# Kernel optimization log

Measured on AMD Instinct MI355X. Metric: run time of the kernel, lower is better.

## Reference

```python
import jax, jax.numpy as jnp
import numpy as np

N, L, S = 512, 1024, 32   # batch, latent dim, spatial (S*S == L)
F = 32 * S * S            # flattened encoder conv features (last conv = 32 ch)
H = 512                   # hidden width of latent MLP heads


def _lrelu(x):
    return jnp.where(x >= 0, x, 0.01 * x)


def _bn(x):
    # BatchNorm2d in training mode, gamma=1, beta=0 (default init)
    m = x.mean((0, 2, 3), keepdims=True)
    v = x.var((0, 2, 3), keepdims=True)
    return (x - m) * jax.lax.rsqrt(v + 1e-5)


def _conv(x, w, b):
    y = jax.lax.conv_general_dilated(x, w, (1, 1), 'SAME',
                                     dimension_numbers=('NCHW', 'OIHW', 'NCHW'))
    return y + b[None, :, None, None]


def _block(x, w, b):
    return _lrelu(_bn(_conv(x, w, b)))


def setup_inputs() -> dict:
    key = jax.random.key(0)
    ks = jax.random.split(key, 16)
    r = lambda k, s, sc: jax.random.normal(k, s, jnp.float32) * sc
    return {
        'x': r(ks[0], (N, 1, S, S), 1.0),
        'eps_c': r(ks[1], (N, L), 1.0),
        'eps_s': r(ks[2], (N, L), 1.0),
        'enc_cw1': r(ks[3], (2, 32, 1, 3, 3), 0.1),   'enc_cb1': jnp.zeros((2, 32)),
        'enc_cw2': r(ks[4], (2, 64, 32, 3, 3), 0.05), 'enc_cb2': jnp.zeros((2, 64)),
        'enc_cw3': r(ks[5], (2, 32, 64, 3, 3), 0.05), 'enc_cb3': jnp.zeros((2, 32)),
        'enc_muW1': r(ks[6], (2, H, F), 0.005), 'enc_muB1': jnp.zeros((2, H)),
        'enc_muW2': r(ks[7], (2, L, H), 0.02),  'enc_muB2': jnp.zeros((2, L)),
        'enc_vaW1': r(ks[8], (2, H, F), 0.005), 'enc_vaB1': jnp.zeros((2, H)),
        'enc_vaW2': r(ks[9], (2, L, H), 0.02),  'enc_vaB2': jnp.zeros((2, L)),
        'dec_cw1': r(ks[10], (2, 32, 1, 3, 3), 0.1),   'dec_cb1': jnp.zeros((2, 32)),
        'dec_cw2': r(ks[11], (2, 64, 32, 3, 3), 0.05), 'dec_cb2': jnp.zeros((2, 64)),
        'dec_cw3': r(ks[12], (2, 1, 64, 3, 3), 0.05),  'dec_cb3': jnp.zeros((2, 1)),
    }


def reference(x, eps_c, eps_s,
              enc_cw1, enc_cb1, enc_cw2, enc_cb2, enc_cw3, enc_cb3,
              enc_muW1, enc_muB1, enc_muW2, enc_muB2,
              enc_vaW1, enc_vaB1, enc_vaW2, enc_vaB2,
              dec_cw1, dec_cb1, dec_cw2, dec_cb2, dec_cw3, dec_cb3):
    def encode(i):
        h = _block(x, enc_cw1[i], enc_cb1[i])
        h = _block(h, enc_cw2[i], enc_cb2[i])
        h = _block(h, enc_cw3[i], enc_cb3[i])
        f = h.reshape(N, -1)                                   # [N, F]
        mu = _lrelu(_lrelu(f @ enc_muW1[i].T + enc_muB1[i]) @ enc_muW2[i].T + enc_muB2[i])
        lv = _lrelu(_lrelu(f @ enc_vaW1[i].T + enc_vaB1[i]) @ enc_vaW2[i].T + enc_vaB2[i])
        return mu, lv                                          # each [N, L]

    def decode(z, i):
        h = z.reshape(N, 1, S, S)
        h = _block(h, dec_cw1[i], dec_cb1[i])
        h = _block(h, dec_cw2[i], dec_cb2[i])
        h = _block(h, dec_cw3[i], dec_cb3[i])
        return h.reshape(N, 1, S, S)

    class_mu, class_logvar = encode(0)
    style_mu, style_logvar = encode(1)

    # precision-weighted product-of-experts group evidence (vectorized)
    precision = jnp.exp(-style_logvar)                  # 1/var, [N, L]
    group_var = 1.0 / precision.sum(0)                  # [L]
    group_mu = (style_mu * precision).sum(0) * group_var  # [L]
    group_logvar = jnp.log(group_var)

    # reparameterize
    z_c = eps_c * jnp.exp(0.5 * class_logvar) + class_mu          # [N, L]
    z_s = eps_s * jnp.exp(0.5 * group_logvar)[None] + group_mu[None]  # [N, L]

    output_c = decode(z_c, 0)
    output_s = jax.nn.relu(decode(z_s, 1))
    output = output_c * output_s                        # [N, 1, S, S]

    kl1 = -0.5 * jnp.sum(1.0 + class_logvar) + 0.5 * (
        jnp.sum(class_mu ** 2) + jnp.sum(jnp.exp(class_logvar) ** 2))
    kl2 = -0.5 * jnp.sum(1.0 + group_logvar) + 0.5 * (
        jnp.sum(group_mu ** 2) + jnp.sum(jnp.exp(group_logvar) ** 2))
    recon = (jnp.exp(x) - jnp.exp(output)) ** 2
    loss = -kl1 + kl2 + recon                           # [N, 1, S, S]
    return loss, output
```

## Files before the change

kernel.cpp:

```cpp
#include <hip/hip_runtime.h>

constexpr int N_   = 512;
constexpr int PIX  = 1024;
constexpr int L_   = 1024;
constexpr int F_   = 32768;
constexpr int H_   = 512;
constexpr float IC_ = 1.0f / (float)(512 * 1024);

__device__ __forceinline__ float lrelu(float t) { return t >= 0.f ? t : 0.01f * t; }

using frag  = __attribute__((ext_vector_type(8))) short;
using f32x4 = __attribute__((ext_vector_type(4))) float;
using s4    = __attribute__((ext_vector_type(4))) short;

__device__ __forceinline__ void split_bf16(float v, short& hi, short& lo) {
    const unsigned b = __float_as_uint(v);
    hi = (short)(b >> 16);
    const float hf = __uint_as_float(b & 0xFFFF0000u);
    lo = (short)(__float_as_uint(v - hf) >> 16);
}

__device__ __forceinline__ frag ld2(const short* p) {
    union { frag f; struct { unsigned long long a, b; } u; } x;
    x.u.a = *(const unsigned long long*)(p);
    x.u.b = *(const unsigned long long*)(p + 4);
    return x.f;
}

__global__ __launch_bounds__(256) void wsplit6_kernel(
    const float* __restrict__ w0, const float* __restrict__ w1,
    const float* __restrict__ w2, const float* __restrict__ w3,
    const float* __restrict__ w4, const float* __restrict__ w5,
    short* __restrict__ hi, short* __restrict__ lo)
{
    const int layer = blockIdx.y;
    const float* W = layer == 0 ? w0 : layer == 1 ? w1 : layer == 2 ? w2 :
                     layer == 3 ? w3 : layer == 4 ? w4 : w5;
    const int CIN  = (layer == 1 || layer == 3) ? 64 : 32;
    const int NCOT = (layer == 1 || layer == 3) ? 2 : 4;
    const int idx = blockIdx.x * 256 + threadIdx.x;
    const int j    = idx & 7;
    const int lane = (idx >> 3) & 63;
    const int q    = lane >> 4, lm = lane & 15;
    const int blk  = idx >> 9;
    const int cot  = blk % NCOT;
    const int rest = blk / NCOT;
    const int pos  = rest % 9;
    const int cc   = rest / 9;
    const int co = cot * 16 + lm;
    const int ci = cc * 32 + q * 8 + j;
    short h, l;
    split_bf16(W[((size_t)co * CIN + ci) * 9 + pos], h, l);
    hi[layer * 18432 + idx] = h;
    lo[layer * 18432 + idx] = l;
}

template<int CIN, int COUT, bool BN_IN>
__global__ __launch_bounds__(256) void conv_mfma(
    const float* __restrict__ in, const short* __restrict__ wh,
    const short* __restrict__ wl, const float* __restrict__ bias,
    float* __restrict__ out, const float* __restrict__ stats_in,
    float* __restrict__ stats_out)
{
    constexpr int NCOT = COUT / 16;
    constexpr int NCH  = CIN / 32;
    constexpr int STR  = 36;
    constexpr int PLsh = 340 * STR;
    __shared__ __align__(16) short hiL[PLsh];
    __shared__ __align__(16) short loL[PLsh];
    __shared__ float red[2 * COUT];
    __shared__ float bnm[64], bni[64];
    const int tid  = threadIdx.x;
    const int n    = blockIdx.x >> 2;
    const int y0   = (blockIdx.x & 3) << 3;
    const int lane = tid & 63;
    const int wv   = tid >> 6;
    const int lm   = lane & 15;
    const int q    = lane >> 4;

    if (tid < 2 * COUT) red[tid] = 0.f;
    if (BN_IN && tid < CIN) {
        const float m  = stats_in[tid] * IC_;
        const float qq = stats_in[CIN + tid] * IC_;
        bnm[tid] = m;
        bni[tid] = rsqrtf(qq - m * m + 1e-5f);
    }
    __syncthreads();

    f32x4 acc[NCOT][4];
#pragma unroll
    for (int t = 0; t < NCOT; ++t)
#pragma unroll
        for (int pt = 0; pt < 4; ++pt) acc[t][pt] = {0.f, 0.f, 0.f, 0.f};

    const int rs0 = tid / 34, cs0 = tid % 34;
    const int idx1 = tid + 256;
    const int rs1 = idx1 / 34, cs1 = idx1 % 34;
    const int gr0 = y0 - 1 + rs0, gc0 = cs0 - 1;
    const int gr1 = y0 - 1 + rs1, gc1 = cs1 - 1;
    const bool in1 = idx1 < 340;
    const bool ok0 = ((unsigned)gr0 < 32u) && ((unsigned)gc0 < 32u);
    const bool ok1 = in1 && ((unsigned)gr1 < 32u) && ((unsigned)gc1 < 32u);
    const int  po0 = gr0 * 32 + gc0;
    const int  po1 = gr1 * 32 + gc1;

    const float* inb = in + ((size_t)n * CIN << 10);

    frag ahA[NCOT], alA[NCOT], ahB[NCOT], alB[NCOT];

    auto LDW = [&](frag (&dh)[NCOT], frag (&dl)[NCOT], int posAbs) {
#pragma unroll
        for (int t = 0; t < NCOT; ++t) {
            const size_t wb = (size_t)((posAbs * NCOT + t) * 512 + lane * 8);
            dh[t] = *(const frag*)&wh[wb];
            dl[t] = *(const frag*)&wl[wb];
        }
    };

    auto COMPUTE = [&](int pos, frag (&fh)[NCOT], frag (&fl)[NCOT]) {
        const int ky = pos / 3, kx = pos - ky * 3;
        __builtin_amdgcn_s_setprio(1);
#pragma unroll
        for (int pt = 0; pt < 4; ++pt) {
            const int ptile = wv * 4 + pt;
            const int row = ptile >> 1;
            const int col = ((ptile & 1) << 4) + lm;
            const int loff = ((row + ky) * 34 + col + kx) * STR + q * 8;
            const frag bh = ld2(&hiL[loff]);
            const frag bl = ld2(&loL[loff]);
#pragma unroll
            for (int t = 0; t < NCOT; ++t) {
                acc[t][pt] = __builtin_amdgcn_mfma_f32_16x16x32_bf16(
                    fh[t], bh, acc[t][pt], 0, 0, 0);
                acc[t][pt] = __builtin_amdgcn_mfma_f32_16x16x32_bf16(
                    fh[t], bl, acc[t][pt], 0, 0, 0);
                acc[t][pt] = __builtin_amdgcn_mfma_f32_16x16x32_bf16(
                    fl[t], bh, acc[t][pt], 0, 0, 0);
            }
        }
        __builtin_amdgcn_s_setprio(0);
    };

#pragma unroll 1
    for (int cc = 0; cc < NCH; ++cc) {
        if (cc) __syncthreads();

        LDW(ahA, alA, cc * 9 + 0);

        {
            float v0r[32], v1r[32];
#pragma unroll
            for (int u = 0; u < 32; ++u) {
                const int cg = cc * 32 + u;
                v0r[u] = ok0 ? inb[((size_t)cg << 10) + po0] : 0.f;
                v1r[u] = ok1 ? inb[((size_t)cg << 10) + po1] : 0.f;
            }
#pragma unroll
            for (int u4 = 0; u4 < 32; u4 += 4) {
                s4 h0v, l0v, h1v, l1v;
#pragma unroll
                for (int e = 0; e < 4; ++e) {
                    const int ci = u4 + e;
                    const int cg = cc * 32 + ci;
                    float v0 = v0r[ci];
                    if (BN_IN && ok0) v0 = lrelu((v0 - bnm[cg]) * bni[cg]);
                    short h, l;
                    split_bf16(v0, h, l);
                    h0v[e] = h; l0v[e] = l;
                    float v1 = v1r[ci];
                    if (BN_IN && ok1) v1 = lrelu((v1 - bnm[cg]) * bni[cg]);
                    short h1, l1;
                    split_bf16(v1, h1, l1);
                    h1v[e] = h1; l1v[e] = l1;
                }
                *(s4*)&hiL[tid * STR + u4] = h0v;
                *(s4*)&loL[tid * STR + u4] = l0v;
                if (in1) {
                    *(s4*)&hiL[idx1 * STR + u4] = h1v;
                    *(s4*)&loL[idx1 * STR + u4] = l1v;
                }
            }
        }
        __syncthreads();

#pragma unroll 1
        for (int pos = 0; pos < 8; pos += 2) {
            LDW(ahB, alB, cc * 9 + pos + 1);
            COMPUTE(pos, ahA, alA);
            LDW(ahA, alA, cc * 9 + pos + 2);
            COMPUTE(pos + 1, ahB, alB);
        }
        COMPUTE(8, ahA, alA);
    }

    float* ob = out + ((size_t)n * COUT << 10);
#pragma unroll
    for (int t = 0; t < NCOT; ++t) {
#pragma unroll
        for (int r = 0; r < 4; ++r) {
            const int co = t * 16 + q * 4 + r;
            const float b = bias[co];
            float s = 0.f, sq = 0.f;
#pragma unroll
            for (int pt = 0; pt < 4; ++pt) {
                const float v = acc[t][pt][r] + b;
                ob[((size_t)co << 10) + (y0 << 5) + ((wv * 4 + pt) << 4) + lm] = v;
                s += v; sq += v * v;
            }
#pragma unroll
            for (int off = 8; off > 0; off >>= 1) {
                s  += __shfl_down(s, off, 64);
                sq += __shfl_down(sq, off, 64);
            }
            if (lm == 0) {
                atomicAdd(&red[co], s);
                atomicAdd(&red[COUT + co], sq);
            }
        }
    }
    __syncthreads();
    if (tid < 2 * COUT) atomicAdd(&stats_out[tid], red[tid]);
}

template<int CIN, int COPB, bool BN_IN>
__global__ __launch_bounds__(256) void conv3x3(
    const float* __restrict__ in, const float* __restrict__ w,
    const float* __restrict__ bias, float* __restrict__ out,
    const float* __restrict__ stats_in, float* __restrict__ stats_out,
    int Cout)
{
    constexpr int CT = (CIN < 4) ? CIN : 4;
    __shared__ float tile[CT * PIX];
    __shared__ float red[2 * COPB];
    const int groups = Cout / COPB;
    const int n   = blockIdx.x / groups;
    const int co0 = (blockIdx.x % groups) * COPB;
    const int tid = threadIdx.x;
    const int x   = tid & 31;
    const int y0  = (tid >> 5) * 4;

    float acc[COPB][4];
#pragma unroll
    for (int c = 0; c < COPB; ++c)
#pragma unroll
        for (int j = 0; j < 4; ++j) acc[c][j] = 0.f;

    const float* inbase = in + (size_t)n * CIN * PIX;

#pragma unroll 1
    for (int s0 = 0; s0 < CIN; s0 += CT) {
        __syncthreads();
#pragma unroll
        for (int s = 0; s < CT; ++s) {
            float4 v = ((const float4*)(inbase + (size_t)(s0 + s) * PIX))[tid];
            if (BN_IN) {
                const int c = s0 + s;
                const float m   = stats_in[c] * IC_;
                const float q   = stats_in[CIN + c] * IC_;
                const float inv = rsqrtf(q - m * m + 1e-5f);
                v.x = lrelu((v.x - m) * inv);
                v.y = lrelu((v.y - m) * inv);
                v.z = lrelu((v.z - m) * inv);
                v.w = lrelu((v.w - m) * inv);
            }
            ((float4*)tile)[s * 256 + tid] = v;
        }
        __syncthreads();
#pragma unroll 2
        for (int s = 0; s < CT; ++s) {
            const int ci = s0 + s;
            const float* tp = tile + s * PIX;
            float r[6][3];
#pragma unroll
            for (int ry = 0; ry < 6; ++ry) {
                const int yy = y0 + ry - 1;
                const bool yok = (unsigned)yy < 32u;
#pragma unroll
                for (int cx = 0; cx < 3; ++cx) {
                    const int xx = x + cx - 1;
                    const bool ok = yok && ((unsigned)xx < 32u);
                    r[ry][cx] = ok ? tp[yy * 32 + xx] : 0.f;
                }
            }
#pragma unroll
            for (int c = 0; c < COPB; ++c) {
                const float* wp = w + ((size_t)(co0 + c) * CIN + ci) * 9;
#pragma unroll
                for (int ky = 0; ky < 3; ++ky)
#pragma unroll
                    for (int kx = 0; kx < 3; ++kx) {
                        const float wv = wp[ky * 3 + kx];
#pragma unroll
                        for (int j = 0; j < 4; ++j)
                            acc[c][j] += r[ky + j][kx] * wv;
                    }
            }
        }
    }

    if (tid < 2 * COPB) red[tid] = 0.f;
    __syncthreads();
#pragma unroll
    for (int c = 0; c < COPB; ++c) {
        const float b = bias[co0 + c];
        float* ob = out + (((size_t)n * Cout + co0 + c) << 10);
        float s = 0.f, q = 0.f;
#pragma unroll
        for (int j = 0; j < 4; ++j) {
            const float v = acc[c][j] + b;
            ob[(y0 + j) * 32 + x] = v;
            s += v; q += v * v;
        }
#pragma unroll
        for (int off = 32; off > 0; off >>= 1) {
            s += __shfl_down(s, off, 64);
            q += __shfl_down(q, off, 64);
        }
        if ((tid & 63) == 0) {
            atomicAdd(&red[c], s);
            atomicAdd(&red[COPB + c], q);
        }
    }
    __syncthreads();
    if (tid < COPB)
        atomicAdd(&stats_out[co0 + tid], red[tid]);
    else if (tid < 2 * COPB)
        atomicAdd(&stats_out[Cout + co0 + tid - COPB], red[tid]);
}

template<bool BN_A>
__global__ __launch_bounds__(256) void gemm_mfma(
    const float* __restrict__ A0, const float* __restrict__ A1,
    const float* __restrict__ B0, const float* __restrict__ B1,
    float* __restrict__ C0, float* __restrict__ C1,
    int K, int Nh, int kchunk, int xph,
    const float* __restrict__ bnstats, int Cin)
{
    __shared__ short AhL[4096], AlL[4096], BhL[4096], BlL[4096];
    const int tid  = threadIdx.x;
    const int head = blockIdx.x / xph;
    const int n0   = (blockIdx.x % xph) * 128;
    const int m0   = blockIdx.y * 128;
    const float* A = head ? A1 : A0;
    const float* B = head ? B1 : B0;
    float*       C = head ? C1 : C0;
    const int k0 = blockIdx.z * kchunk;
    const int k1 = k0 + kchunk;

    const int lane = tid & 63;
    const int wv   = tid >> 6;
    const int wm   = wv & 1;
    const int wn   = wv >> 1;
    const int lm   = lane & 15;
    const int q    = lane >> 4;

    const int srow = tid >> 1;
    const int smt  = srow >> 4;
    const int slm  = srow & 15;
    const int sq0  = (tid & 1) * 2;
    const int ks   = (tid & 1) * 16;

    float bn_m = 0.f, bn_inv = 1.f;
    if (BN_A) {
        const int c = k0 >> 10;
        bn_m = bnstats[c] * IC_;
        const float qq = bnstats[Cin + c] * IC_;
        bn_inv = rsqrtf(qq - bn_m * bn_m + 1e-5f);
    }

    f32x4 acc[4][4];
#pragma unroll
    for (int i = 0; i < 4; ++i)
#pragma unroll
        for (int j = 0; j < 4; ++j) acc[i][j] = {0.f, 0.f, 0.f, 0.f};

    auto cv8 = [](float4 u, float4 w2, frag& h, frag& l) {
        const float v[8] = {u.x, u.y, u.z, u.w, w2.x, w2.y, w2.z, w2.w};
#pragma unroll
        for (int e = 0; e < 8; ++e) {
            short hh, ll;
            split_bf16(v[e], hh, ll);
            h[e] = hh; l[e] = ll;
        }
    };

    float4 a4[4], b4[4];
    auto LOADAB = [&](int kb) {
        const float* Ap = A + (size_t)(m0 + srow) * K + kb + ks;
        const float* Bp = B + (size_t)(n0 + srow) * K + kb + ks;
#pragma unroll
        for (int g = 0; g < 4; ++g) a4[g] = ((const float4*)Ap)[g];
#pragma unroll
        for (int g = 0; g < 4; ++g) b4[g] = ((const float4*)Bp)[g];
    };

    LOADAB(k0);

#pragma unroll 1
    for (int kb = k0; kb < k1; kb += 32) {
        if (BN_A) {
#pragma unroll
            for (int g = 0; g < 4; ++g) {
                a4[g].x = lrelu((a4[g].x - bn_m) * bn_inv);
                a4[g].y = lrelu((a4[g].y - bn_m) * bn_inv);
                a4[g].z = lrelu((a4[g].z - bn_m) * bn_inv);
                a4[g].w = lrelu((a4[g].w - bn_m) * bn_inv);
            }
        }

        frag ah0, al0, ah1, al1, bh0, bl0, bh1, bl1;
        cv8(a4[0], a4[1], ah0, al0);
        cv8(a4[2], a4[3], ah1, al1);
        cv8(b4[0], b4[1], bh0, bl0);
        cv8(b4[2], b4[3], bh1, bl1);

        __syncthreads();
        const int o0 = ((smt * 4 + sq0) * 16 + slm) * 8;
        const int o1 = ((smt * 4 + sq0 + 1) * 16 + slm) * 8;
        *(frag*)&AhL[o0] = ah0;  *(frag*)&AhL[o1] = ah1;
        *(frag*)&AlL[o0] = al0;  *(frag*)&AlL[o1] = al1;
        *(frag*)&BhL[o0] = bh0;  *(frag*)&BhL[o1] = bh1;
        *(frag*)&BlL[o0] = bl0;  *(frag*)&BlL[o1] = bl1;
        __syncthreads();

        frag fah[4], fal[4], fbh[4], fbl[4];
#pragma unroll
        for (int t = 0; t < 4; ++t) {
            const int oa = (((wm * 4 + t) * 4 + q) * 16 + lm) * 8;
            const int ob = (((wn * 4 + t) * 4 + q) * 16 + lm) * 8;
            fah[t] = *(const frag*)&AhL[oa];
            fal[t] = *(const frag*)&AlL[oa];
            fbh[t] = *(const frag*)&BhL[ob];
            fbl[t] = *(const frag*)&BlL[ob];
        }

        if (kb + 32 < k1) LOADAB(kb + 32);

#pragma unroll
        for (int i = 0; i < 4; ++i)
#pragma unroll
            for (int j = 0; j < 4; ++j) {
                acc[i][j] = __builtin_amdgcn_mfma_f32_16x16x32_bf16(
                    fah[i], fbh[j], acc[i][j], 0, 0, 0);
                acc[i][j] = __builtin_amdgcn_mfma_f32_16x16x32_bf16(
                    fah[i], fbl[j], acc[i][j], 0, 0, 0);
                acc[i][j] = __builtin_amdgcn_mfma_f32_16x16x32_bf16(
                    fal[i], fbh[j], acc[i][j], 0, 0, 0);
            }
    }

#pragma unroll
    for (int i = 0; i < 4; ++i) {
        const int m = m0 + wm * 64 + i * 16 + q * 4;
#pragma unroll
        for (int j = 0; j < 4; ++j) {
            const int n = n0 + wn * 64 + j * 16 + lm;
            float* cp = C + (size_t)m * Nh + n;
#pragma unroll
            for (int r = 0; r < 4; ++r)
                atomicAdd(cp + (size_t)r * Nh, acc[i][j][r]);
        }
    }
}

__global__ __launch_bounds__(256) void bias_lrelu2_kernel(
    float* __restrict__ bufa, const float* __restrict__ ba,
    float* __restrict__ bufb, const float* __restrict__ bb,
    int Nn, int per)
{
    const int idx = blockIdx.x * 256 + threadIdx.x;
    if (idx < per) {
        bufa[idx] = lrelu(bufa[idx] + ba[idx % Nn]);
    } else {
        const int j = idx - per;
        bufb[j] = lrelu(bufb[j] + bb[j % Nn]);
    }
}

__device__ __forceinline__ void block_reduce_atomic(float t, float* target)
{
#pragma unroll
    for (int off = 32; off > 0; off >>= 1) t += __shfl_down(t, off, 64);
    __shared__ float lt[4];
    const int wave = threadIdx.x >> 6, lane = threadIdx.x & 63;
    if (lane == 0) lt[wave] = t;
    __syncthreads();
    if (threadIdx.x == 0) atomicAdd(target, lt[0] + lt[1] + lt[2] + lt[3]);
}

__global__ __launch_bounds__(256) void poe_kernel(
    const float* __restrict__ mu1, const float* __restrict__ lv1,
    float* __restrict__ gmu, float* __restrict__ glv, float* __restrict__ kl)
{
    const int l = blockIdx.x * 256 + threadIdx.x;
    float sp = 0.f, sm = 0.f;
    for (int n = 0; n < N_; ++n) {
        const float lv = lv1[(size_t)n * L_ + l];
        const float p  = expf(-lv);
        sp += p;
        sm += mu1[(size_t)n * L_ + l] * p;
    }
    const float gv = 1.f / sp;
    const float gm = sm * gv;
    const float gl = -logf(sp);
    gmu[l] = gm;
    glv[l] = gl;
    const float t = -0.5f * (1.f + gl) + 0.5f * (gm * gm + gv * gv);
    block_reduce_atomic(t, &kl[1]);
}

__global__ __launch_bounds__(256) void reparam_kernel(
    const float* __restrict__ mu0, const float* __restrict__ lv0,
    const float* __restrict__ eps_c, const float* __restrict__ eps_s,
    const float* __restrict__ gmu, const float* __restrict__ glv,
    float* __restrict__ zc, float* __restrict__ zs, float* __restrict__ kl)
{
    const int idx = blockIdx.x * 256 + threadIdx.x;
    const int l = idx & (L_ - 1);
    const float m  = mu0[idx];
    const float lv = lv0[idx];
    zc[idx] = eps_c[idx] * expf(0.5f * lv) + m;
    zs[idx] = eps_s[idx] * expf(0.5f * glv[l]) + gmu[l];
    const float e = expf(lv);
    const float t = -0.5f * (1.f + lv) + 0.5f * (m * m + e * e);
    block_reduce_atomic(t, &kl[0]);
}

__global__ __launch_bounds__(256) void final_kernel(
    const float* __restrict__ x, const float* __restrict__ oc,
    const float* __restrict__ os, const float* __restrict__ stC,
    const float* __restrict__ stS, const float* __restrict__ kl,
    float* __restrict__ out)
{
    const int idx = blockIdx.x * 256 + threadIdx.x;
    const float mc = stC[0] * IC_, qc = stC[1] * IC_;
    const float ivc = rsqrtf(qc - mc * mc + 1e-5f);
    const float ms = stS[0] * IC_, qs = stS[1] * IC_;
    const float ivs = rsqrtf(qs - ms * ms + 1e-5f);
    const float tc = lrelu((oc[idx] - mc) * ivc);
    const float ts = fmaxf((os[idx] - ms) * ivs, 0.f);
    const float o = tc * ts;
    const float d = expf(x[idx]) - expf(o);
    out[idx]            = -kl[0] + kl[1] + d * d;
    out[N_ * PIX + idx] = o;
}

extern "C" void kernel_launch(void* const* d_in, const int* in_sizes, int n_in,
                              void* d_out, int out_size, void* d_ws, size_t ws_size,
                              hipStream_t stream)
{
    const float* x        = (const float*)d_in[0];
    const float* eps_c    = (const float*)d_in[1];
    const float* eps_s    = (const float*)d_in[2];
    const float* enc_cw1  = (const float*)d_in[3];
    const float* enc_cb1  = (const float*)d_in[4];
    const float* enc_cw2  = (const float*)d_in[5];
    const float* enc_cb2  = (const float*)d_in[6];
    const float* enc_cw3  = (const float*)d_in[7];
    const float* enc_cb3  = (const float*)d_in[8];
    const float* enc_muW1 = (const float*)d_in[9];
    const float* enc_muB1 = (const float*)d_in[10];
    const float* enc_muW2 = (const float*)d_in[11];
    const float* enc_muB2 = (const float*)d_in[12];
    const float* enc_vaW1 = (const float*)d_in[13];
    const float* enc_vaB1 = (const float*)d_in[14];
    const float* enc_vaW2 = (const float*)d_in[15];
    const float* enc_vaB2 = (const float*)d_in[16];
    const float* dec_cw1  = (const float*)d_in[17];
    const float* dec_cb1  = (const float*)d_in[18];
    const float* dec_cw2  = (const float*)d_in[19];
    const float* dec_cb2  = (const float*)d_in[20];
    const float* dec_cw3  = (const float*)d_in[21];
    const float* dec_cb3  = (const float*)d_in[22];
    float* out = (float*)d_out;

    float* ws   = (float*)d_ws;
    float* bufA = ws;
    float* bufB = bufA + (size_t)N_ * 64 * PIX;
    float* h1   = bufB + (size_t)N_ * 32 * PIX;
    float* h2   = h1 + N_ * H_;
    float* mu0  = h2 + N_ * H_;
    float* lv0  = mu0 + N_ * L_;
    float* mu1  = lv0 + N_ * L_;
    float* lv1  = mu1 + N_ * L_;
    float* zc   = lv1 + N_ * L_;
    float* zs   = zc + N_ * L_;
    float* oc   = zs + N_ * L_;
    float* os   = oc + N_ * L_;
    float* gmu  = os + N_ * L_;
    float* glv  = gmu + L_;
    float* stats = glv + L_;
    float* kl   = stats + 12 * 128;
    short* wsh  = (short*)(kl + 4);
    short* wsl  = wsh + 6 * 18432;

    auto st  = [&](int s) { return stats + 128 * s; };
    auto whp = [&](int layer) { return wsh + layer * 18432; };
    auto wlp = [&](int layer) { return wsl + layer * 18432; };

    hipMemsetAsync(stats, 0, (12 * 128 + 4) * sizeof(float), stream);

    wsplit6_kernel<<<dim3(72, 6), 256, 0, stream>>>(
        enc_cw2, enc_cw3, enc_cw2 + 64 * 32 * 9, enc_cw3 + 32 * 64 * 9,
        dec_cw2, dec_cw2 + 64 * 32 * 9, wsh, wsl);

    for (int i = 0; i < 2; ++i) {
        const float* cw1 = enc_cw1 + (size_t)i * 32 * 9;
        const float* cb1 = enc_cb1 + (size_t)i * 32;
        const float* cb2 = enc_cb2 + (size_t)i * 64;
        const float* cb3 = enc_cb3 + (size_t)i * 32;

        conv3x3<1, 16, false><<<N_ * 2, 256, 0, stream>>>(
            x, cw1, cb1, bufB, nullptr, st(i * 3 + 0), 32);
        conv_mfma<32, 64, true><<<N_ * 4, 256, 0, stream>>>(
            bufB, whp(i * 2), wlp(i * 2), cb2, bufA, st(i * 3 + 0), st(i * 3 + 1));
        conv_mfma<64, 32, true><<<N_ * 4, 256, 0, stream>>>(
            bufA, whp(i * 2 + 1), wlp(i * 2 + 1), cb3, bufB, st(i * 3 + 1), st(i * 3 + 2));

        const float* W1m = enc_muW1 + (size_t)i * H_ * F_;
        const float* B1m = enc_muB1 + (size_t)i * H_;
        const float* W2m = enc_muW2 + (size_t)i * L_ * H_;
        const float* B2m = enc_muB2 + (size_t)i * L_;
        const float* W1v = enc_vaW1 + (size_t)i * H_ * F_;
        const float* B1v = enc_vaB1 + (size_t)i * H_;
        const float* W2v = enc_vaW2 + (size_t)i * L_ * H_;
        const float* B2v = enc_vaB2 + (size_t)i * L_;
        float* mu_i = (i == 0) ? mu0 : mu1;
        float* lv_i = (i == 0) ? lv0 : lv1;

        hipMemsetAsync(h1, 0, (size_t)2 * N_ * H_ * sizeof(float), stream);
        gemm_mfma<true><<<dim3(8, 4, 32), 256, 0, stream>>>(
            bufB, bufB, W1m, W1v, h1, h2, F_, H_, 1024, 4, st(i * 3 + 2), 32);
        bias_lrelu2_kernel<<<(2 * N_ * H_) / 256, 256, 0, stream>>>(
            h1, B1m, h2, B1v, H_, N_ * H_);

        hipMemsetAsync(mu_i, 0, (size_t)2 * N_ * L_ * sizeof(float), stream);
        gemm_mfma<false><<<dim3(16, 4, 8), 256, 0, stream>>>(
            h1, h2, W2m, W2v, mu_i, lv_i, H_, L_, 64, 8, nullptr, 0);
        bias_lrelu2_kernel<<<(2 * N_ * L_) / 256, 256, 0, stream>>>(
            mu_i, B2m, lv_i, B2v, L_, N_ * L_);
    }

    poe_kernel<<<L_ / 256, 256, 0, stream>>>(mu1, lv1, gmu, glv, kl);
    reparam_kernel<<<(N_ * L_) / 256, 256, 0, stream>>>(
        mu0, lv0, eps_c, eps_s, gmu, glv, zc, zs, kl);

    for (int i = 0; i < 2; ++i) {
        const float* cw1 = dec_cw1 + (size_t)i * 32 * 9;
        const float* cb1 = dec_cb1 + (size_t)i * 32;
        const float* cb2 = dec_cb2 + (size_t)i * 64;
        const float* cw3 = dec_cw3 + (size_t)i * 64 * 9;
        const float* cb3 = dec_cb3 + (size_t)i * 1;
        const float* zi = (i == 0) ? zc : zs;
        float* oi = (i == 0) ? oc : os;

        conv3x3<1, 16, false><<<N_ * 2, 256, 0, stream>>>(
            zi, cw1, cb1, bufB, nullptr, st(6 + i * 3 + 0), 32);
        conv_mfma<32, 64, true><<<N_ * 4, 256, 0, stream>>>(
            bufB, whp(4 + i), wlp(4 + i), cb2, bufA, st(6 + i * 3 + 0), st(6 + i * 3 + 1));
        conv3x3<64, 1, true><<<N_, 256, 0, stream>>>(
            bufA, cw3, cb3, oi, st(6 + i * 3 + 1), st(6 + i * 3 + 2), 1);
    }

    final_kernel<<<(N_ * PIX) / 256, 256, 0, stream>>>(
        x, oc, os, st(8), st(11), kl, out);
}
```

Before: 1.527 ms.

## Double-buffer GEMM global loads, use lighter barriers, halve split-K count

The GEMM kernel now keeps two register buffers of A/B tiles and issues the prefetch for the step after next before the LDS write barrier, so global loads have more time in flight. The split-K chunk is doubled, which halves the z-grid and the atomicAdd traffic. Because a chunk now spans two BN channels, two sets of BN stats are computed. __syncthreads is replaced by a barrier that waits only on LDS counters, which avoids draining outstanding global loads. The cost is more register pressure and less grid parallelism.

```diff
diff --git a/kernel.cpp b/kernel.cpp
--- a/kernel.cpp
+++ b/kernel.cpp
@@ -12,6 +12,12 @@
 using frag  = __attribute__((ext_vector_type(8))) short;
 using f32x4 = __attribute__((ext_vector_type(4))) float;
 using s4    = __attribute__((ext_vector_type(4))) short;
+
+#define BAR() do {                                              \
+    asm volatile("s_waitcnt lgkmcnt(0)" ::: "memory");          \
+    __builtin_amdgcn_s_barrier();                               \
+    asm volatile("" ::: "memory");                              \
+} while (0)
 
 __device__ __forceinline__ void split_bf16(float v, short& hi, short& lo) {
     const unsigned b = __float_as_uint(v);
@@ -143,7 +149,7 @@
 
 #pragma unroll 1
     for (int cc = 0; cc < NCH; ++cc) {
-        if (cc) __syncthreads();
+        if (cc) BAR();
 
         LDW(ahA, alA, cc * 9 + 0);
 
@@ -181,7 +187,7 @@
                 }
             }
         }
-        __syncthreads();
+        BAR();
 
 #pragma unroll 1
         for (int pos = 0; pos < 8; pos += 2) {
@@ -360,12 +366,16 @@
     const int sq0  = (tid & 1) * 2;
     const int ks   = (tid & 1) * 16;
 
-    float bn_m = 0.f, bn_inv = 1.f;
+    float bnm0 = 0.f, bni0 = 1.f, bnm1 = 0.f, bni1 = 1.f;
     if (BN_A) {
-        const int c = k0 >> 10;
-        bn_m = bnstats[c] * IC_;
-        const float qq = bnstats[Cin + c] * IC_;
-        bn_inv = rsqrtf(qq - bn_m * bn_m + 1e-5f);
+        const int c0 = k0 >> 10;
+        bnm0 = bnstats[c0] * IC_;
+        const float q0 = bnstats[Cin + c0] * IC_;
+        bni0 = rsqrtf(q0 - bnm0 * bnm0 + 1e-5f);
+        const int c1 = (c0 + 1 < Cin) ? c0 + 1 : c0;
+        bnm1 = bnstats[c1] * IC_;
+        const float q1 = bnstats[Cin + c1] * IC_;
+        bni1 = rsqrtf(q1 - bnm1 * bnm1 + 1e-5f);
     }
 
     f32x4 acc[4][4];
@@ -384,8 +394,9 @@
         }
     };
 
-    float4 a4[4], b4[4];
-    auto LOADAB = [&](int kb) {
+    float4 aA[4], bA[4], aB[4], bB[4];
+
+    auto LOADAB = [&](float4 (&a4)[4], float4 (&b4)[4], int kb) {
         const float* Ap = A + (size_t)(m0 + srow) * K + kb + ks;
         const float* Bp = B + (size_t)(n0 + srow) * K + kb + ks;
 #pragma unroll
@@ -394,17 +405,17 @@
         for (int g = 0; g < 4; ++g) b4[g] = ((const float4*)Bp)[g];
     };
 
-    LOADAB(k0);
-
-#pragma unroll 1
-    for (int kb = k0; kb < k1; kb += 32) {
+    auto STEP = [&](float4 (&a4)[4], float4 (&b4)[4], int kb, int kpf) {
         if (BN_A) {
+            const int sel = (kb - k0) >> 10;
+            const float m   = sel ? bnm1 : bnm0;
+            const float inv = sel ? bni1 : bni0;
 #pragma unroll
             for (int g = 0; g < 4; ++g) {
-                a4[g].x = lrelu((a4[g].x - bn_m) * bn_inv);
-                a4[g].y = lrelu((a4[g].y - bn_m) * bn_inv);
-                a4[g].z = lrelu((a4[g].z - bn_m) * bn_inv);
-                a4[g].w = lrelu((a4[g].w - bn_m) * bn_inv);
+                a4[g].x = lrelu((a4[g].x - m) * inv);
+                a4[g].y = lrelu((a4[g].y - m) * inv);
+                a4[g].z = lrelu((a4[g].z - m) * inv);
+                a4[g].w = lrelu((a4[g].w - m) * inv);
             }
         }
 
@@ -414,14 +425,16 @@
         cv8(b4[0], b4[1], bh0, bl0);
         cv8(b4[2], b4[3], bh1, bl1);
 
-        __syncthreads();
+        if (kpf < k1) LOADAB(a4, b4, kpf);
+
+        BAR();
         const int o0 = ((smt * 4 + sq0) * 16 + slm) * 8;
         const int o1 = ((smt * 4 + sq0 + 1) * 16 + slm) * 8;
         *(frag*)&AhL[o0] = ah0;  *(frag*)&AhL[o1] = ah1;
         *(frag*)&AlL[o0] = al0;  *(frag*)&AlL[o1] = al1;
         *(frag*)&BhL[o0] = bh0;  *(frag*)&BhL[o1] = bh1;
         *(frag*)&BlL[o0] = bl0;  *(frag*)&BlL[o1] = bl1;
-        __syncthreads();
+        BAR();
 
         frag fah[4], fal[4], fbh[4], fbl[4];
 #pragma unroll
@@ -434,8 +447,6 @@
             fbl[t] = *(const frag*)&BlL[ob];
         }
 
-        if (kb + 32 < k1) LOADAB(kb + 32);
-
 #pragma unroll
         for (int i = 0; i < 4; ++i)
 #pragma unroll
@@ -447,6 +458,15 @@
                 acc[i][j] = __builtin_amdgcn_mfma_f32_16x16x32_bf16(
                     fal[i], fbh[j], acc[i][j], 0, 0, 0);
             }
+    };
+
+    LOADAB(aA, bA, k0);
+    LOADAB(aB, bB, k0 + 32);
+
+#pragma unroll 1
+    for (int kb = k0; kb < k1; kb += 64) {
+        STEP(aA, bA, kb,      kb + 64);
+        STEP(aB, bB, kb + 32, kb + 96);
     }
 
 #pragma unroll
@@ -629,14 +649,14 @@
         float* lv_i = (i == 0) ? lv0 : lv1;
 
         hipMemsetAsync(h1, 0, (size_t)2 * N_ * H_ * sizeof(float), stream);
-        gemm_mfma<true><<<dim3(8, 4, 32), 256, 0, stream>>>(
-            bufB, bufB, W1m, W1v, h1, h2, F_, H_, 1024, 4, st(i * 3 + 2), 32);
+        gemm_mfma<true><<<dim3(8, 4, 16), 256, 0, stream>>>(
+            bufB, bufB, W1m, W1v, h1, h2, F_, H_, 2048, 4, st(i * 3 + 2), 32);
         bias_lrelu2_kernel<<<(2 * N_ * H_) / 256, 256, 0, stream>>>(
             h1, B1m, h2, B1v, H_, N_ * H_);
 
         hipMemsetAsync(mu_i, 0, (size_t)2 * N_ * L_ * sizeof(float), stream);
-        gemm_mfma<false><<<dim3(16, 4, 8), 256, 0, stream>>>(
-            h1, h2, W2m, W2v, mu_i, lv_i, H_, L_, 64, 8, nullptr, 0);
+        gemm_mfma<false><<<dim3(16, 4, 4), 256, 0, stream>>>(
+            h1, h2, W2m, W2v, mu_i, lv_i, H_, L_, 128, 8, nullptr, 0);
         bias_lrelu2_kernel<<<(2 * N_ * L_) / 256, 256, 0, stream>>>(
             mu_i, B2m, lv_i, B2v, L_, N_ * L_);
     }
```

After: 1.460 ms. 1.05x faster.
